# Kernel optimization log

Measured on AMD Instinct MI355X. Metric: run time of the kernel, lower is better.

Reference implementation:

```python
import jax, jax.numpy as jnp
import numpy as np

H, C = 4, 32          # heads, per-head channels (hidden=128)
NEG_SLOPE = 0.2        # PyG GATv2Conv default LeakyReLU slope


def setup_inputs() -> dict:
    key = jax.random.key(0)
    ks = jax.random.split(key, 9)
    N_a, N_m = 100000, 50000     # asset / market node counts
    E_aa, E_am = 600000, 400000  # edge counts per edge type
    D, L = 128, 2                # hidden dims, num GAT layers
    sc = 1.0 / np.sqrt(D).astype(np.float32)

    x_asset = jax.random.normal(ks[0], (N_a, D), jnp.float32)
    x_market = jax.random.normal(ks[1], (N_m, D), jnp.float32)

    edge_aa = jax.random.randint(ks[2], (2, E_aa), 0, N_a, jnp.int32)
    src_am = jax.random.randint(ks[3], (E_am,), 0, N_a, jnp.int32)
    dst_am = jax.random.randint(ks[4], (E_am,), 0, N_m, jnp.int32)
    edge_am = jnp.stack([src_am, dst_am])

    Wl = jax.random.normal(ks[5], (L, D, D), jnp.float32) * sc   # lin_l (src)
    Wr = jax.random.normal(ks[6], (L, D, D), jnp.float32) * sc   # lin_r (dst)
    att = jax.random.normal(ks[7], (L, H, C), jnp.float32) * sc  # attention vector
    bias = jnp.zeros((L, D), jnp.float32)

    return {"x_asset": x_asset, "x_market": x_market,
            "edge_aa": edge_aa, "edge_am": edge_am,
            "Wl": Wl, "Wr": Wr, "att": att, "bias": bias}


def _gatv2(x_src, x_dst, src, dst, Wl, Wr, att, bias):
    """One GATv2Conv: gather-attend-scatter. x_src:[Ns,D], x_dst:[Nd,D]."""
    N_dst = x_dst.shape[0]
    xl = (x_src @ Wl).reshape(-1, H, C)   # transformed src (messages)
    xr = (x_dst @ Wr).reshape(-1, H, C)   # transformed dst
    z = jax.nn.leaky_relu(xl[src] + xr[dst], NEG_SLOPE)     # [E,H,C]
    e = jnp.einsum('ehc,hc->eh', z, att)                    # [E,H] scores
    # softmax over incoming edges per destination node
    m = jax.lax.stop_gradient(jax.ops.segment_max(e, dst, num_segments=N_dst))
    w = jnp.exp(e - m[dst])
    s = jax.ops.segment_sum(w, dst, num_segments=N_dst)
    alpha = w / jnp.maximum(s[dst], jnp.float32(1e-16))     # [E,H]
    out = jax.ops.segment_sum(alpha[..., None] * xl[src], dst, num_segments=N_dst)
    return out.reshape(N_dst, H * C) + bias


def reference(x_asset, x_market, edge_aa, edge_am, Wl, Wr, att, bias):
    # Faithful to source: x_dict is never updated between layers, so every
    # layer reads the ORIGINAL features and only the last layer's dict is kept.
    L = Wl.shape[0]
    out_asset = out_market = None
    for l in range(L):
        out_asset = _gatv2(x_asset, x_asset, edge_aa[0], edge_aa[1],
                           Wl[l], Wr[l], att[l], bias[l])
        out_market = _gatv2(x_asset, x_market, edge_am[0], edge_am[1],
                            Wl[l], Wr[l], att[l], bias[l])
    return out_asset, out_market
```

## Files before the change

kernel.cpp:

```cpp
#include <hip/hip_runtime.h>
#include <hip/hip_bf16.h>


#define NEG_SLOPE 0.2f

typedef __attribute__((ext_vector_type(8))) short short8;
typedef __attribute__((ext_vector_type(4))) float floatx4;
typedef __attribute__((ext_vector_type(4))) unsigned short us4;

__device__ inline unsigned short f2bf(float x) {
    union { float f; unsigned u; } v; v.f = x;
    unsigned r = v.u + 0x7FFF + ((v.u >> 16) & 1);
    return (unsigned short)(r >> 16);
}
__device__ inline float bf2f(unsigned short h) {
    union { unsigned u; float f; } v; v.u = (unsigned)h << 16;
    return v.f;
}

__device__ inline void stage_w(const float* __restrict__ W, unsigned char* lds, int t) {
    const int n = t & 127;
    const int kh = t >> 7;
    unsigned short hb[32], lb[32];
#pragma unroll
    for (int i = 0; i < 32; ++i) {
        int k = kh * 32 + i;
        float w = W[(size_t)k * 128 + n];
        unsigned short h = f2bf(w);
        hb[i] = h;
        lb[i] = f2bf(w - bf2f(h));
    }
#pragma unroll
    for (int j = 0; j < 4; ++j) {
        int koff = (kh * 32 + j * 8) * 2;
        int off = ((n * 256 + koff) ^ ((n & 15) << 4));
        short8 hv, lv;
#pragma unroll
        for (int i = 0; i < 8; ++i) { hv[i] = (short)hb[j * 8 + i]; lv[i] = (short)lb[j * 8 + i]; }
        *(short8*)(&lds[off]) = hv;
        *(short8*)(&lds[32768 + off]) = lv;
    }
}

__device__ inline void mfma_pass(const unsigned char* lds, const short8* ah,
                                 const short8* al, int lr, int lkb, floatx4* acc) {
#pragma unroll
    for (int ks = 0; ks < 4; ++ks) {
#pragma unroll
        for (int ct = 0; ct < 8; ++ct) {
            int n = ct * 16 + lr;
            int off = ((n * 256 + (ks * 32 + lkb) * 2) ^ ((n & 15) << 4));
            short8 bh = *(const short8*)(&lds[off]);
            short8 bl = *(const short8*)(&lds[32768 + off]);
            acc[ct] = __builtin_amdgcn_mfma_f32_16x16x32_bf16(ah[ks], bh, acc[ct], 0, 0, 0);
            acc[ct] = __builtin_amdgcn_mfma_f32_16x16x32_bf16(al[ks], bh, acc[ct], 0, 0, 0);
            acc[ct] = __builtin_amdgcn_mfma_f32_16x16x32_bf16(ah[ks], bl, acc[ct], 0, 0, 0);
        }
    }
}

__global__ __launch_bounds__(512) void gemm_all(const float* __restrict__ Xa,
                                                const float* __restrict__ Xm,
                                                const float* __restrict__ Wl,
                                                const float* __restrict__ Wr,
                                                unsigned short* __restrict__ XLb,
                                                float* __restrict__ XR,
                                                int Na, int Nm, int nblkA) {
    __shared__ __align__(16) unsigned char lds[65536];

    const int t = threadIdx.x;
    const int wv = t >> 6;
    const int l = t & 63;
    const int lr = l & 15;
    const int lkb = (l >> 4) * 8;
    const bool isA = ((int)blockIdx.x < nblkA);
    const int blk = isA ? blockIdx.x : blockIdx.x - nblkA;
    const float* __restrict__ X = isA ? Xa : Xm;
    const int M = isA ? Na : Nm;
    const int arow = blk * 128 + wv * 16 + lr;

    short8 ah[4], al[4];
    if (arow < M) {
#pragma unroll
        for (int ks = 0; ks < 4; ++ks) {
            const float* xp = X + (size_t)arow * 128 + ks * 32 + lkb;
            float4 f0 = *(const float4*)xp;
            float4 f1 = *(const float4*)(xp + 4);
            float xv[8] = {f0.x, f0.y, f0.z, f0.w, f1.x, f1.y, f1.z, f1.w};
            short8 h, lo;
#pragma unroll
            for (int i = 0; i < 8; ++i) {
                unsigned short hb = f2bf(xv[i]);
                h[i] = (short)hb;
                lo[i] = (short)f2bf(xv[i] - bf2f(hb));
            }
            ah[ks] = h; al[ks] = lo;
        }
    } else {
#pragma unroll
        for (int ks = 0; ks < 4; ++ks) { ah[ks] = (short8)0; al[ks] = (short8)0; }
    }

    const int orow0 = blk * 128 + wv * 16 + (l >> 4) * 4;
    floatx4 acc[8];

    if (isA) {
        stage_w(Wl, lds, t);
        __syncthreads();
#pragma unroll
        for (int ct = 0; ct < 8; ++ct) acc[ct] = (floatx4)0.f;
        mfma_pass(lds, ah, al, lr, lkb, acc);
#pragma unroll
        for (int ct = 0; ct < 8; ++ct) {
            int col = ct * 16 + lr;
#pragma unroll
            for (int r = 0; r < 4; ++r) {
                int orow = orow0 + r;
                if (orow < M) XLb[(size_t)orow * 128 + col] = f2bf(acc[ct][r]);
            }
        }
        __syncthreads();
        stage_w(Wr, lds, t);
        __syncthreads();
#pragma unroll
        for (int ct = 0; ct < 8; ++ct) acc[ct] = (floatx4)0.f;
        mfma_pass(lds, ah, al, lr, lkb, acc);
#pragma unroll
        for (int ct = 0; ct < 8; ++ct) {
            int col = ct * 16 + lr;
#pragma unroll
            for (int r = 0; r < 4; ++r) {
                int orow = orow0 + r;
                if (orow < M) XR[(size_t)orow * 128 + col] = acc[ct][r];
            }
        }
    } else {
        stage_w(Wr, lds, t);
        __syncthreads();
#pragma unroll
        for (int ct = 0; ct < 8; ++ct) acc[ct] = (floatx4)0.f;
        mfma_pass(lds, ah, al, lr, lkb, acc);
        float* __restrict__ XRm = XR + (size_t)Na * 128;
#pragma unroll
        for (int ct = 0; ct < 8; ++ct) {
            int col = ct * 16 + lr;
#pragma unroll
            for (int r = 0; r < 4; ++r) {
                int orow = orow0 + r;
                if (orow < M) XRm[(size_t)orow * 128 + col] = acc[ct][r];
            }
        }
    }
}

__global__ void degcount(const int* __restrict__ aadst, const int* __restrict__ amdst,
                         int* __restrict__ deg, int Eaa, int Eam, int Na) {
    const int nqaa = Eaa >> 2, nqam = Eam >> 2;
    int i = blockIdx.x * 256 + threadIdx.x;
    if (i < nqaa) {
        int4 d = ((const int4*)aadst)[i];
        atomicAdd(&deg[d.x], 1); atomicAdd(&deg[d.y], 1);
        atomicAdd(&deg[d.z], 1); atomicAdd(&deg[d.w], 1);
    } else if (i < nqaa + nqam) {
        int4 d = ((const int4*)amdst)[i - nqaa];
        atomicAdd(&deg[Na + d.x], 1); atomicAdd(&deg[Na + d.y], 1);
        atomicAdd(&deg[Na + d.z], 1); atomicAdd(&deg[Na + d.w], 1);
    } else {
        int k = i - (nqaa + nqam);
        int remaa = Eaa & 3, remam = Eam & 3;
        if (k < remaa) atomicAdd(&deg[aadst[nqaa * 4 + k]], 1);
        else if (k - remaa < remam) atomicAdd(&deg[Na + amdst[nqam * 4 + k - remaa]], 1);
    }
}

__global__ void alloc_seg(const int* __restrict__ deg, int* __restrict__ row_start,
                          int* __restrict__ fill, int* __restrict__ cursor, int N) {
    int i = blockIdx.x * 256 + threadIdx.x;
    if (i < N) {
        int d = deg[i];
        int r = atomicAdd(cursor, d);
        row_start[i] = r;
        fill[i] = r;
    }
}

__global__ void fillcsr(const int* __restrict__ aasrc, const int* __restrict__ aadst,
                        const int* __restrict__ amsrc, const int* __restrict__ amdst,
                        int* __restrict__ fill, int* __restrict__ csr,
                        int Eaa, int Eam, int Na) {
    const int nqaa = Eaa >> 2, nqam = Eam >> 2;
    int i = blockIdx.x * 256 + threadIdx.x;
    if (i < nqaa) {
        int4 sv = ((const int4*)aasrc)[i];
        int4 dv = ((const int4*)aadst)[i];
        csr[atomicAdd(&fill[dv.x], 1)] = sv.x;
        csr[atomicAdd(&fill[dv.y], 1)] = sv.y;
        csr[atomicAdd(&fill[dv.z], 1)] = sv.z;
        csr[atomicAdd(&fill[dv.w], 1)] = sv.w;
    } else if (i < nqaa + nqam) {
        int4 sv = ((const int4*)amsrc)[i - nqaa];
        int4 dv = ((const int4*)amdst)[i - nqaa];
        csr[atomicAdd(&fill[Na + dv.x], 1)] = sv.x;
        csr[atomicAdd(&fill[Na + dv.y], 1)] = sv.y;
        csr[atomicAdd(&fill[Na + dv.z], 1)] = sv.z;
        csr[atomicAdd(&fill[Na + dv.w], 1)] = sv.w;
    } else {
        int k = i - (nqaa + nqam);
        int remaa = Eaa & 3, remam = Eam & 3;
        if (k < remaa)
            csr[atomicAdd(&fill[aadst[nqaa * 4 + k]], 1)] = aasrc[nqaa * 4 + k];
        else if (k - remaa < remam)
            csr[atomicAdd(&fill[Na + amdst[nqam * 4 + k - remaa]], 1)] = amsrc[nqam * 4 + k - remaa];
    }
}

__global__ __launch_bounds__(256) void gather_gat(const unsigned short* __restrict__ XLb,
                                                  const int* __restrict__ csr,
                                                  const int* __restrict__ row_start,
                                                  const int* __restrict__ deg,
                                                  const float* __restrict__ att,
                                                  const float* __restrict__ bias,
                                                  float* __restrict__ out,
                                                  int Ntot) {
    int wid = (blockIdx.x * 256 + threadIdx.x) >> 6;
    const int l = threadIdx.x & 63;
    if (wid >= Ntot) return;
    const int half = l >> 5;
    const int q = l & 31;

    const float4 av = *(const float4*)(att + (q >> 3) * 32 + (q & 7) * 4);
    const float4 xr = *(const float4*)(out + (size_t)wid * 128 + q * 4);

    const int beg = row_start[wid];
    const int end = beg + deg[wid];
    float s = 0.f;
    float4 acc = make_float4(0.f, 0.f, 0.f, 0.f);

#define EDGE(rv, act)                                                        \
    {                                                                        \
        float x0 = bf2f(rv[0]), x1 = bf2f(rv[1]), x2 = bf2f(rv[2]), x3 = bf2f(rv[3]); \
        float z0 = x0 + xr.x; z0 = fmaxf(z0, NEG_SLOPE * z0);                \
        float z1 = x1 + xr.y; z1 = fmaxf(z1, NEG_SLOPE * z1);                \
        float z2 = x2 + xr.z; z2 = fmaxf(z2, NEG_SLOPE * z2);                \
        float z3 = x3 + xr.w; z3 = fmaxf(z3, NEG_SLOPE * z3);                \
        float p = z0 * av.x;                                                 \
        p = fmaf(z1, av.y, p);                                               \
        p = fmaf(z2, av.z, p);                                               \
        p = fmaf(z3, av.w, p);                                               \
        p += __shfl_xor(p, 1);                                               \
        p += __shfl_xor(p, 2);                                               \
        p += __shfl_xor(p, 4);                                               \
        float w = (act) ? __expf(p) : 0.f;                                   \
        s += w;                                                              \
        acc.x = fmaf(w, x0, acc.x);                                          \
        acc.y = fmaf(w, x1, acc.y);                                          \
        acc.z = fmaf(w, x2, acc.z);                                          \
        acc.w = fmaf(w, x3, acc.w);                                          \
    }

    for (int j = beg; j < end; j += 8) {
        const int b = j + half * 4;
        const bool a0 = (b + 0) < end, a1 = (b + 1) < end,
                   a2 = (b + 2) < end, a3 = (b + 3) < end;
        int s0 = csr[a0 ? b + 0 : beg];
        int s1 = csr[a1 ? b + 1 : beg];
        int s2 = csr[a2 ? b + 2 : beg];
        int s3 = csr[a3 ? b + 3 : beg];
        const us4 r0 = *(const us4*)(XLb + (size_t)s0 * 128 + q * 4);
        const us4 r1 = *(const us4*)(XLb + (size_t)s1 * 128 + q * 4);
        const us4 r2 = *(const us4*)(XLb + (size_t)s2 * 128 + q * 4);
        const us4 r3 = *(const us4*)(XLb + (size_t)s3 * 128 + q * 4);
        EDGE(r0, a0);
        EDGE(r1, a1);
        EDGE(r2, a2);
        EDGE(r3, a3);
    }
#undef EDGE

    s += __shfl_xor(s, 32);
    acc.x += __shfl_xor(acc.x, 32);
    acc.y += __shfl_xor(acc.y, 32);
    acc.z += __shfl_xor(acc.z, 32);
    acc.w += __shfl_xor(acc.w, 32);

    if (half == 0) {
        float inv = 1.f / fmaxf(s, 1e-16f);
        const float4 bv = *(const float4*)(bias + q * 4);
        float4 o = make_float4(fmaf(acc.x, inv, bv.x), fmaf(acc.y, inv, bv.y),
                               fmaf(acc.z, inv, bv.z), fmaf(acc.w, inv, bv.w));
        *(float4*)(out + (size_t)wid * 128 + q * 4) = o;
    }
}

extern "C" void kernel_launch(void* const* d_in, const int* in_sizes, int n_in,
                              void* d_out, int out_size, void* d_ws, size_t ws_size,
                              hipStream_t stream) {
    const float* x_asset  = (const float*)d_in[0];
    const float* x_market = (const float*)d_in[1];
    const int*   eaa      = (const int*)d_in[2];
    const int*   eam      = (const int*)d_in[3];
    const float* Wl       = (const float*)d_in[4];
    const float* Wr       = (const float*)d_in[5];
    const float* att      = (const float*)d_in[6];
    const float* bias     = (const float*)d_in[7];

    const int Na  = in_sizes[0] / 128;
    const int Nm  = in_sizes[1] / 128;
    const int Eaa = in_sizes[2] / 2;
    const int Eam = in_sizes[3] / 2;
    const int Ntot = Na + Nm;

    const float* Wl1   = Wl + 128 * 128;
    const float* Wr1   = Wr + 128 * 128;
    const float* att1  = att + 128;
    const float* bias1 = bias + 128;

    unsigned short* XLb = (unsigned short*)d_ws;
    int*   deg = (int*)(XLb + (size_t)Na * 128);
    int*   cursor = deg + Ntot;
    int*   fill = cursor + 1;
    int*   row_start = fill + Ntot;
    int*   csr = row_start + Ntot;

    float* XR = (float*)d_out;

    hipMemsetAsync(deg, 0, sizeof(int) * (size_t)(Ntot + 1), stream);

    const int nq = (Eaa >> 2) + (Eam >> 2) + 8;
    degcount<<<(nq + 255) / 256, 256, 0, stream>>>(eaa + Eaa, eam + Eam, deg, Eaa, Eam, Na);

    const int nblkA = (Na + 127) / 128;
    const int nblkM = (Nm + 127) / 128;
    gemm_all<<<nblkA + nblkM, 512, 0, stream>>>(x_asset, x_market, Wl1, Wr1,
                                                XLb, XR, Na, Nm, nblkA);

    alloc_seg<<<(Ntot + 255) / 256, 256, 0, stream>>>(deg, row_start, fill, cursor, Ntot);

    fillcsr<<<(nq + 255) / 256, 256, 0, stream>>>(eaa, eaa + Eaa, eam, eam + Eam,
                                                  fill, csr, Eaa, Eam, Na);

    gather_gat<<<(Ntot * 64 + 255) / 256, 256, 0, stream>>>(
        XLb, csr, row_start, deg, att1, bias1, (float*)d_out, Ntot);
}
```

Baseline: 384.6 us.

## Fuse CSR construction into one persistent kernel with grid barriers

Result: slower. 595.7 us (+54.9%).

```diff
diff --git a/kernel.cpp b/kernel.cpp
--- a/kernel.cpp
+++ b/kernel.cpp
@@ -153,66 +153,79 @@
     }
 }
 
-__global__ void degcount(const int* __restrict__ aadst, const int* __restrict__ amdst,
-                         int* __restrict__ deg, int Eaa, int Eam, int Na) {
+#define GBAR(idx)                                                            \
+    __syncthreads();                                                         \
+    if (threadIdx.x == 0) {                                                  \
+        __threadfence();                                                     \
+        atomicAdd(&bars[idx], 1);                                            \
+        while (atomicAdd(&bars[idx], 0) < (int)gridDim.x)                    \
+            __builtin_amdgcn_s_sleep(16);                                    \
+        __threadfence();                                                     \
+    }                                                                        \
+    __syncthreads();
+
+__global__ __launch_bounds__(256) void csr_build(
+        const int* __restrict__ aasrc, const int* __restrict__ aadst,
+        const int* __restrict__ amsrc, const int* __restrict__ amdst,
+        int* __restrict__ deg, int* __restrict__ cursor,
+        int* __restrict__ row_start, int* __restrict__ fill,
+        int* __restrict__ csr, int* __restrict__ bars,
+        int Eaa, int Eam, int Na, int Ntot) {
+    const int nthr = gridDim.x * 256;
+    const int tid = blockIdx.x * 256 + threadIdx.x;
     const int nqaa = Eaa >> 2, nqam = Eam >> 2;
-    int i = blockIdx.x * 256 + threadIdx.x;
-    if (i < nqaa) {
-        int4 d = ((const int4*)aadst)[i];
-        atomicAdd(&deg[d.x], 1); atomicAdd(&deg[d.y], 1);
-        atomicAdd(&deg[d.z], 1); atomicAdd(&deg[d.w], 1);
-    } else if (i < nqaa + nqam) {
-        int4 d = ((const int4*)amdst)[i - nqaa];
-        atomicAdd(&deg[Na + d.x], 1); atomicAdd(&deg[Na + d.y], 1);
-        atomicAdd(&deg[Na + d.z], 1); atomicAdd(&deg[Na + d.w], 1);
-    } else {
-        int k = i - (nqaa + nqam);
-        int remaa = Eaa & 3, remam = Eam & 3;
-        if (k < remaa) atomicAdd(&deg[aadst[nqaa * 4 + k]], 1);
-        else if (k - remaa < remam) atomicAdd(&deg[Na + amdst[nqam * 4 + k - remaa]], 1);
-    }
-}
-
-__global__ void alloc_seg(const int* __restrict__ deg, int* __restrict__ row_start,
-                          int* __restrict__ fill, int* __restrict__ cursor, int N) {
-    int i = blockIdx.x * 256 + threadIdx.x;
-    if (i < N) {
-        int d = deg[i];
+    const int remaa = Eaa & 3, remam = Eam & 3;
+    const int nitems = nqaa + nqam + remaa + remam;
+
+    for (int i = tid; i < nitems; i += nthr) {
+        if (i < nqaa) {
+            int4 d = ((const int4*)aadst)[i];
+            atomicAdd(&deg[d.x], 1); atomicAdd(&deg[d.y], 1);
+            atomicAdd(&deg[d.z], 1); atomicAdd(&deg[d.w], 1);
+        } else if (i < nqaa + nqam) {
+            int4 d = ((const int4*)amdst)[i - nqaa];
+            atomicAdd(&deg[Na + d.x], 1); atomicAdd(&deg[Na + d.y], 1);
+            atomicAdd(&deg[Na + d.z], 1); atomicAdd(&deg[Na + d.w], 1);
+        } else {
+            int k = i - nqaa - nqam;
+            if (k < remaa) atomicAdd(&deg[aadst[nqaa * 4 + k]], 1);
+            else atomicAdd(&deg[Na + amdst[nqam * 4 + (k - remaa)]], 1);
+        }
+    }
+    GBAR(0)
+    for (int i = tid; i < Ntot; i += nthr) {
+        int d = atomicAdd(&deg[i], 0);
         int r = atomicAdd(cursor, d);
         row_start[i] = r;
         fill[i] = r;
     }
-}
-
-__global__ void fillcsr(const int* __restrict__ aasrc, const int* __restrict__ aadst,
-                        const int* __restrict__ amsrc, const int* __restrict__ amdst,
-                        int* __restrict__ fill, int* __restrict__ csr,
-                        int Eaa, int Eam, int Na) {
-    const int nqaa = Eaa >> 2, nqam = Eam >> 2;
-    int i = blockIdx.x * 256 + threadIdx.x;
-    if (i < nqaa) {
-        int4 sv = ((const int4*)aasrc)[i];
-        int4 dv = ((const int4*)aadst)[i];
-        csr[atomicAdd(&fill[dv.x], 1)] = sv.x;
-        csr[atomicAdd(&fill[dv.y], 1)] = sv.y;
-        csr[atomicAdd(&fill[dv.z], 1)] = sv.z;
-        csr[atomicAdd(&fill[dv.w], 1)] = sv.w;
-    } else if (i < nqaa + nqam) {
-        int4 sv = ((const int4*)amsrc)[i - nqaa];
-        int4 dv = ((const int4*)amdst)[i - nqaa];
-        csr[atomicAdd(&fill[Na + dv.x], 1)] = sv.x;
-        csr[atomicAdd(&fill[Na + dv.y], 1)] = sv.y;
-        csr[atomicAdd(&fill[Na + dv.z], 1)] = sv.z;
-        csr[atomicAdd(&fill[Na + dv.w], 1)] = sv.w;
-    } else {
-        int k = i - (nqaa + nqam);
-        int remaa = Eaa & 3, remam = Eam & 3;
-        if (k < remaa)
-            csr[atomicAdd(&fill[aadst[nqaa * 4 + k]], 1)] = aasrc[nqaa * 4 + k];
-        else if (k - remaa < remam)
-            csr[atomicAdd(&fill[Na + amdst[nqam * 4 + k - remaa]], 1)] = amsrc[nqam * 4 + k - remaa];
-    }
-}
+    GBAR(1)
+    for (int i = tid; i < nitems; i += nthr) {
+        if (i < nqaa) {
+            int4 sv = ((const int4*)aasrc)[i];
+            int4 dv = ((const int4*)aadst)[i];
+            csr[atomicAdd(&fill[dv.x], 1)] = sv.x;
+            csr[atomicAdd(&fill[dv.y], 1)] = sv.y;
+            csr[atomicAdd(&fill[dv.z], 1)] = sv.z;
+            csr[atomicAdd(&fill[dv.w], 1)] = sv.w;
+        } else if (i < nqaa + nqam) {
+            int4 sv = ((const int4*)amsrc)[i - nqaa];
+            int4 dv = ((const int4*)amdst)[i - nqaa];
+            csr[atomicAdd(&fill[Na + dv.x], 1)] = sv.x;
+            csr[atomicAdd(&fill[Na + dv.y], 1)] = sv.y;
+            csr[atomicAdd(&fill[Na + dv.z], 1)] = sv.z;
+            csr[atomicAdd(&fill[Na + dv.w], 1)] = sv.w;
+        } else {
+            int k = i - nqaa - nqam;
+            if (k < remaa)
+                csr[atomicAdd(&fill[aadst[nqaa * 4 + k]], 1)] = aasrc[nqaa * 4 + k];
+            else
+                csr[atomicAdd(&fill[Na + amdst[nqam * 4 + (k - remaa)]], 1)] =
+                    amsrc[nqam * 4 + (k - remaa)];
+        }
+    }
+}
+#undef GBAR
 
 __global__ __launch_bounds__(256) void gather_gat(const unsigned short* __restrict__ XLb,
                                                   const int* __restrict__ csr,
@@ -227,12 +240,15 @@
     if (wid >= Ntot) return;
     const int half = l >> 5;
     const int q = l & 31;
+    const unsigned qo = (unsigned)q * 8u;
+    const unsigned char* __restrict__ XLB = (const unsigned char*)XLb;
 
     const float4 av = *(const float4*)(att + (q >> 3) * 32 + (q & 7) * 4);
     const float4 xr = *(const float4*)(out + (size_t)wid * 128 + q * 4);
 
     const int beg = row_start[wid];
     const int end = beg + deg[wid];
+    const int last = end - 1;
     float s = 0.f;
     float4 acc = make_float4(0.f, 0.f, 0.f, 0.f);
 
@@ -260,20 +276,18 @@
 
     for (int j = beg; j < end; j += 8) {
         const int b = j + half * 4;
-        const bool a0 = (b + 0) < end, a1 = (b + 1) < end,
-                   a2 = (b + 2) < end, a3 = (b + 3) < end;
-        int s0 = csr[a0 ? b + 0 : beg];
-        int s1 = csr[a1 ? b + 1 : beg];
-        int s2 = csr[a2 ? b + 2 : beg];
-        int s3 = csr[a3 ? b + 3 : beg];
-        const us4 r0 = *(const us4*)(XLb + (size_t)s0 * 128 + q * 4);
-        const us4 r1 = *(const us4*)(XLb + (size_t)s1 * 128 + q * 4);
-        const us4 r2 = *(const us4*)(XLb + (size_t)s2 * 128 + q * 4);
-        const us4 r3 = *(const us4*)(XLb + (size_t)s3 * 128 + q * 4);
-        EDGE(r0, a0);
-        EDGE(r1, a1);
-        EDGE(r2, a2);
-        EDGE(r3, a3);
+        int s0 = csr[min(b + 0, last)];
+        int s1 = csr[min(b + 1, last)];
+        int s2 = csr[min(b + 2, last)];
+        int s3 = csr[min(b + 3, last)];
+        const us4 r0 = *(const us4*)(XLB + (((unsigned)s0 << 8) + qo));
+        const us4 r1 = *(const us4*)(XLB + (((unsigned)s1 << 8) + qo));
+        const us4 r2 = *(const us4*)(XLB + (((unsigned)s2 << 8) + qo));
+        const us4 r3 = *(const us4*)(XLB + (((unsigned)s3 << 8) + qo));
+        EDGE(r0, (b + 0) < end);
+        EDGE(r1, (b + 1) < end);
+        EDGE(r2, (b + 2) < end);
+        EDGE(r3, (b + 3) < end);
     }
 #undef EDGE
 
@@ -318,27 +332,24 @@
     unsigned short* XLb = (unsigned short*)d_ws;
     int*   deg = (int*)(XLb + (size_t)Na * 128);
     int*   cursor = deg + Ntot;
-    int*   fill = cursor + 1;
+    int*   bars = cursor + 1;
+    int*   fill = bars + 8;
     int*   row_start = fill + Ntot;
     int*   csr = row_start + Ntot;
 
     float* XR = (float*)d_out;
 
-    hipMemsetAsync(deg, 0, sizeof(int) * (size_t)(Ntot + 1), stream);
-
-    const int nq = (Eaa >> 2) + (Eam >> 2) + 8;
-    degcount<<<(nq + 255) / 256, 256, 0, stream>>>(eaa + Eaa, eam + Eam, deg, Eaa, Eam, Na);
+    hipMemsetAsync(deg, 0, sizeof(int) * (size_t)(Ntot + 9), stream);
+
+    csr_build<<<1024, 256, 0, stream>>>(eaa, eaa + Eaa, eam, eam + Eam,
+                                        deg, cursor, row_start, fill, csr, bars,
+                                        Eaa, Eam, Na, Ntot);
 
     const int nblkA = (Na + 127) / 128;
     const int nblkM = (Nm + 127) / 128;
     gemm_all<<<nblkA + nblkM, 512, 0, stream>>>(x_asset, x_market, Wl1, Wr1,
                                                 XLb, XR, Na, Nm, nblkA);
 
-    alloc_seg<<<(Ntot + 255) / 256, 256, 0, stream>>>(deg, row_start, fill, cursor, Ntot);
-
-    fillcsr<<<(nq + 255) / 256, 256, 0, stream>>>(eaa, eaa + Eaa, eam, eam + Eam,
-                                                  fill, csr, Eaa, Eam, Na);
-
     gather_gat<<<(Ntot * 64 + 255) / 256, 256, 0, stream>>>(
         XLb, csr, row_start, deg, att1, bias1, (float*)d_out, Ntot);
 }
```
